# Performance work log

Hardware: AMD Instinct MI355X
Metric: run time of the kernel (lower is better)

Reference implementation:

```python
import jax, jax.numpy as jnp
import numpy as np

N_IMG = 256; N_PAD = 512; N_DELAYS = 32; N_GRID = 512
PIX = 4e-5; L_IMG = N_IMG * PIX
R_BODY = 0.008; V0 = 1500.0; GRID_HALF = 0.02
N_TH = 240; N_INT = 250; W0 = 30.0
LAM_TV = 1e-3; LAM_L1 = 1e-3

def _fourier_coord(n, l):
    f = np.fft.fftshift(np.fft.fftfreq(n, d=l / n))
    kx, ky = np.meshgrid(f, f, indexing='ij')
    k = 2.0 * np.pi * np.sqrt(kx ** 2 + ky ** 2)
    theta = np.mod(np.arctan2(ky, kx), 2.0 * np.pi)
    return k.astype(np.float32), theta.astype(np.float32)

_K2D, _TH2D = _fourier_coord(N_PAD, 2.0 * L_IMG)
K2D = jnp.asarray(_K2D)[None, None]            # [1,1,P,P]
TH2D = jnp.asarray(_TH2D)                      # [P,P]
MASK0 = jnp.asarray(((_TH2D >= 0.0) & (_TH2D <= 2 * np.pi)).astype(np.float32))
_THPI = np.mod(_TH2D + np.pi, 2 * np.pi)
MASK1 = jnp.asarray(((_THPI >= 0.0) & (_THPI <= 2 * np.pi)).astype(np.float32))
K_LOSS = jnp.asarray(np.fft.ifftshift(_K2D))[None, None]
_SIG = 0.0015 / PIX / np.sqrt(2.0 * np.log(2.0))   # gaussian window sigma (pixels)
_AX = np.arange(N_IMG) - (N_IMG - 1) / 2.0
_G = np.exp(-_AX ** 2 / (2.0 * _SIG ** 2))
GWIN = jnp.asarray(np.outer(_G, _G).astype(np.float32))[None]   # [1,N,N]
THETAS_WF = jnp.linspace(0.0, 2.0 * np.pi, N_TH, dtype=jnp.float32)   # [T]
STEPS = jnp.linspace(0.0, 1.0, N_INT, dtype=jnp.float32)[None]        # [1,S]


def _interp1d(xg, yg, xn):
    # linear interp on uniform grid xg (1D) of values yg; xn arbitrary shape
    dxg = xg[1] - xg[0]
    t = (xn - xg[0]) / dxg
    f = jnp.clip(jnp.floor(t).astype(jnp.int32), 0, xg.shape[0] - 1)
    c = jnp.clip(jnp.ceil(t).astype(jnp.int32), 0, xg.shape[0] - 1)
    yf, yc = yg[f], yg[c]
    denom = jnp.where(c == f, 1.0, xg[c] - xg[f])
    lin = yf + (yc - yf) * (xn - xg[f]) / denom
    return jnp.where(c == f, yc, lin)


def _wavefront(xq, yq, SoS, x_vec, y_vec):
    # time-of-flight wavefront: trapezoid quadrature of (1 - v0/SoS) along rays
    r = jnp.sqrt(xq ** 2 + yq ** 2)
    phi = jnp.arctan2(xq, yq)
    th = THETAS_WF[:, None]                      # [T,1]
    s = jnp.sin(th - phi)
    cd = jnp.cos(th - phi)                       # cos(phi - th) == cos(th - phi)
    disc = jnp.maximum(R_BODY ** 2 - (r * s) ** 2, 0.0)
    l_in = jnp.sqrt(disc) + r * cd
    l_out = 2.0 * jnp.sqrt(disc) * (cd >= 0.0).astype(jnp.float32)
    l = jnp.where(r < R_BODY, l_in, l_out)       # [T,1]
    dx = x_vec[1] - x_vec[0]
    dy = y_vec[1] - y_vec[0]
    xi = jnp.round((xq - l * STEPS * jnp.sin(th) - x_vec[0]) / dx).astype(jnp.int32)
    yi = jnp.round((yq - l * STEPS * jnp.cos(th) - y_vec[0]) / dy).astype(jnp.int32)
    fint = 1.0 - V0 / SoS[(-yi) % N_GRID, xi % N_GRID]   # [T,S] gather
    xs = l * STEPS                               # [T,S]
    wf = jnp.sum(0.5 * (fint[:, 1:] + fint[:, :-1]) * (xs[:, 1:] - xs[:, :-1]), axis=1)
    return THETAS_WF, wf


def _tf_pact(delays, thetas, wfs):
    w = _interp1d(thetas, wfs, TH2D)
    w_pi = _interp1d(thetas, wfs, jnp.mod(TH2D + jnp.pi, 2.0 * jnp.pi))
    d = delays.reshape(1, -1, 1, 1)
    tf = (jnp.exp(-1j * K2D * (d - w)) * MASK0 + jnp.exp(1j * K2D * (d - w_pi)) * MASK1) * 0.5
    return jnp.fft.ifftshift(tf, axes=(-2, -1))  # [1,D,P,P] complex


def _siren(x, W1, b1, W2, b2, W3, b3, W4, b4):
    h = jnp.sin(W0 * (x @ W1 + b1))
    h = jnp.sin(W0 * (h @ W2 + b2))
    h = jnp.sin(W0 * (h @ W3 + b3))
    return h @ W4 + b4


def _forward(W1, b1, W2, b2, W3, b3, W4, b4, y_img, delays, xq, yq,
             mgrid_masked, mask, mask_idx, x_vec, y_vec):
    out = _siren(mgrid_masked, W1, b1, W2, b2, W3, b3, W4, b4)[:, 0]
    SoS = jnp.full((N_GRID * N_GRID,), 1499.363, jnp.float32)
    SoS = SoS.at[mask_idx].set(out * 170.0 + 1550.0).reshape(N_GRID, N_GRID)
    thetas, wfs = _wavefront(xq[0], yq[0], SoS, x_vec, y_vec)
    H = _tf_pact(delays, thetas, wfs)
    yw = y_img * GWIN                                  # [1,D,N,N]
    pad = N_IMG // 2
    yp = jnp.pad(yw, ((0, 0), (0, 0), (pad, pad), (pad, pad)))
    Y = jnp.fft.fft2(jnp.fft.ifftshift(yp, axes=(-2, -1)))
    Ht = jnp.conj(H)
    HtH = jnp.abs(H) ** 2
    rhs = jnp.sum(Y * Ht, axis=-3, keepdims=True)
    lhs = jnp.sum(HtH, axis=-3, keepdims=True)
    X = rhs / lhs
    x_rec = jnp.fft.fftshift(jnp.fft.ifft2(X), axes=(-2, -1)).real
    data = jnp.mean((jnp.abs(Y) * K_LOSS - jnp.abs(H * X) * K_LOSS) ** 2, axis=(-3, -2, -1))
    tv = LAM_TV * (jnp.sum(jnp.abs((SoS[1:, :] - SoS[:-1, :]) * mask[1:, :]))
                   + jnp.sum(jnp.abs((SoS[:, 1:] - SoS[:, :-1]) * mask[:, 1:])))
    l1 = LAM_L1 * jnp.mean(jnp.abs(SoS - 1550.0) * mask)
    loss = data + tv + l1
    return x_rec, SoS, loss


def setup_inputs() -> dict:
    key = jax.random.key(0)
    ks = jax.random.split(key, 12)
    xg = np.linspace(-GRID_HALF, GRID_HALF, N_GRID).astype(np.float32)
    XX, YY = np.meshgrid(xg, xg, indexing='ij')
    mask_np = (XX ** 2 + YY ** 2 <= R_BODY ** 2).astype(np.float32)
    mask_idx = np.nonzero(mask_np.reshape(-1))[0].astype(np.int32)
    lin = np.linspace(-1.0, 1.0, N_GRID).astype(np.float32)
    GX, GY = np.meshgrid(lin, lin, indexing='ij')
    mgrid = np.stack([GX, GY], axis=-1).reshape(-1, 2)
    H = 128
    c = np.sqrt(6.0 / H) / W0
    def u(k, shape, b):
        return jax.random.uniform(k, shape, jnp.float32, -b, b)
    return {
        'W1': u(ks[0], (2, H), 0.5), 'b1': u(ks[1], (H,), 0.5),
        'W2': u(ks[2], (H, H), c), 'b2': u(ks[3], (H,), c),
        'W3': u(ks[4], (H, H), c), 'b3': u(ks[5], (H,), c),
        'W4': u(ks[6], (H, 1), c), 'b4': u(ks[7], (1,), c),
        'y_img': jax.random.normal(ks[8], (1, N_DELAYS, N_IMG, N_IMG), jnp.float32),
        'delays': jax.random.normal(ks[9], (N_DELAYS,), jnp.float32) * 5e-4,
        'xq': jnp.array([0.002], jnp.float32),
        'yq': jnp.array([0.001], jnp.float32),
        'mgrid_masked': jnp.asarray(mgrid[mask_idx]),
        'mask': jnp.asarray(mask_np),
        'mask_idx': jnp.asarray(mask_idx),
        'x_vec': jnp.asarray(xg),
        'y_vec': jnp.asarray(xg),
    }


def reference(W1, b1, W2, b2, W3, b3, W4, b4, y_img, delays, xq, yq,
              mgrid_masked, mask, mask_idx, x_vec, y_vec):
    return _forward(W1, b1, W2, b2, W3, b3, W4, b4, y_img, delays, xq, yq,
                    mgrid_masked, mask, mask_idx, x_vec, y_vec)
```

## Files before the change

### kernel.cpp

```cpp
#include <hip/hip_runtime.h>
#include <hip/hip_bf16.h>
#include <math.h>

#define NP 512
#define NIMG 256
#define NDEL 32
#define NTH 240
#define NINT 250
#define SOS_ELEMS (512*512)
#define MLP_P 32
#define PHY(i) ((i) + ((i) >> 3))
#define RSW 576
#define PI_F 3.14159265358979323846f

__device__ __forceinline__ int brev9(int i) { return (int)(__brev((unsigned)i) >> 23); }

__device__ __forceinline__ float block_reduce_any(float v) {
  #pragma unroll
  for (int o = 32; o > 0; o >>= 1) v += __shfl_down(v, o, 64);
  __shared__ float red[16];
  int lane = threadIdx.x & 63, wid = threadIdx.x >> 6;
  __syncthreads();
  if (lane == 0) red[wid] = v;
  __syncthreads();
  float r = 0.f;
  if (threadIdx.x == 0) {
    int nw = blockDim.x >> 6;
    for (int i = 0; i < nw; ++i) r += red[i];
  }
  return r;
}

__device__ __forceinline__ void r4_bfly(float2& x0, float2& x1, float2& x2, float2& x3,
                                        float c1, float s1n, float c2, float s2n, float sign) {
  float t1x = x1.x * c1 - x1.y * s1n, t1y = x1.x * s1n + x1.y * c1;
  float y0x = x0.x + t1x, y0y = x0.y + t1y;
  float y1x = x0.x - t1x, y1y = x0.y - t1y;
  float t3x = x3.x * c1 - x3.y * s1n, t3y = x3.x * s1n + x3.y * c1;
  float y2x = x2.x + t3x, y2y = x2.y + t3y;
  float y3x = x2.x - t3x, y3y = x2.y - t3y;
  float t2x = y2x * c2 - y2y * s2n, t2y = y2x * s2n + y2y * c2;
  float ux = y3x * c2 - y3y * s2n, uy = y3x * s2n + y3y * c2;
  float t4x = -sign * uy, t4y = sign * ux;
  x0 = make_float2(y0x + t2x, y0y + t2y);
  x2 = make_float2(y0x - t2x, y0y - t2y);
  x1 = make_float2(y1x + t4x, y1y + t4y);
  x3 = make_float2(y1x - t4x, y1y - t4y);
}

__device__ __forceinline__ void fft512_r4_fwd_rows(float2 (*s)[RSW], int lt) {
  #pragma unroll
  for (int pass = 0; pass < 4; ++pass) {
    const int sh = 2 * pass;
    const int h = 1 << sh;
    int p = lt & 127;
    int rbase = (lt >> 7) << 2;
    int j = p & (h - 1);
    int g = p >> sh;
    int base = (g << (sh + 2)) + j;
    int i0 = PHY(base), i1 = PHY(base + h), i2 = PHY(base + 2 * h), i3 = PHY(base + 3 * h);
    float ang1 = -PI_F * (float)j / (float)h;
    float s1n, c1; __sincosf(ang1, &s1n, &c1);
    float s2n, c2; __sincosf(0.5f * ang1, &s2n, &c2);
    #pragma unroll
    for (int rr = 0; rr < 4; ++rr) {
      int r = rbase + rr;
      float2 x0 = s[r][i0], x1 = s[r][i1], x2 = s[r][i2], x3 = s[r][i3];
      r4_bfly(x0, x1, x2, x3, c1, s1n, c2, s2n, -1.f);
      s[r][i0] = x0; s[r][i1] = x1; s[r][i2] = x2; s[r][i3] = x3;
    }
    __syncthreads();
  }
  {
    int p = lt;
    int i1 = PHY(p), i2 = PHY(p + 256);
    float ang = -PI_F * (float)p * (1.f / 256.f);
    float sn, cs; __sincosf(ang, &sn, &cs);
    #pragma unroll
    for (int r = 0; r < 8; ++r) {
      float2 a = s[r][i1], b = s[r][i2];
      float tr = b.x * cs - b.y * sn;
      float ti = b.x * sn + b.y * cs;
      s[r][i1] = make_float2(a.x + tr, a.y + ti);
      s[r][i2] = make_float2(a.x - tr, a.y - ti);
    }
    __syncthreads();
  }
}

__device__ __forceinline__ void fft512_r4_fwd_rows4(float2 (*s)[RSW], int tid) {
  #pragma unroll
  for (int pass = 0; pass < 4; ++pass) {
    const int sh = 2 * pass;
    const int h = 1 << sh;
    int p = tid & 127;
    int rbase = (tid >> 7) << 1;
    int j = p & (h - 1);
    int g = p >> sh;
    int base = (g << (sh + 2)) + j;
    int i0 = PHY(base), i1 = PHY(base + h), i2 = PHY(base + 2 * h), i3 = PHY(base + 3 * h);
    float ang1 = -PI_F * (float)j / (float)h;
    float s1n, c1; __sincosf(ang1, &s1n, &c1);
    float s2n, c2; __sincosf(0.5f * ang1, &s2n, &c2);
    #pragma unroll
    for (int rr = 0; rr < 2; ++rr) {
      int r = rbase + rr;
      float2 x0 = s[r][i0], x1 = s[r][i1], x2 = s[r][i2], x3 = s[r][i3];
      r4_bfly(x0, x1, x2, x3, c1, s1n, c2, s2n, -1.f);
      s[r][i0] = x0; s[r][i1] = x1; s[r][i2] = x2; s[r][i3] = x3;
    }
    __syncthreads();
  }
  {
    int p = tid;
    int i1 = PHY(p), i2 = PHY(p + 256);
    float ang = -PI_F * (float)p * (1.f / 256.f);
    float sn, cs; __sincosf(ang, &sn, &cs);
    #pragma unroll
    for (int r = 0; r < 4; ++r) {
      float2 a = s[r][i1], b = s[r][i2];
      float tr = b.x * cs - b.y * sn;
      float ti = b.x * sn + b.y * cs;
      s[r][i1] = make_float2(a.x + tr, a.y + ti);
      s[r][i2] = make_float2(a.x - tr, a.y - ti);
    }
    __syncthreads();
  }
}

__device__ __forceinline__ void fft512_r4_row(float2* s, int tid, float sign) {
  #pragma unroll
  for (int pass = 0; pass < 4; ++pass) {
    const int sh = 2 * pass;
    const int h = 1 << sh;
    if (tid < 128) {
      int j = tid & (h - 1);
      int g = tid >> sh;
      int base = (g << (sh + 2)) + j;
      int i0 = PHY(base), i1 = PHY(base + h), i2 = PHY(base + 2 * h), i3 = PHY(base + 3 * h);
      float ang1 = sign * PI_F * (float)j / (float)h;
      float s1n, c1; __sincosf(ang1, &s1n, &c1);
      float s2n, c2; __sincosf(0.5f * ang1, &s2n, &c2);
      float2 x0 = s[i0], x1 = s[i1], x2 = s[i2], x3 = s[i3];
      r4_bfly(x0, x1, x2, x3, c1, s1n, c2, s2n, sign);
      s[i0] = x0; s[i1] = x1; s[i2] = x2; s[i3] = x3;
    }
    __syncthreads();
  }
  {
    int i1 = PHY(tid), i2 = PHY(tid + 256);
    float ang = sign * PI_F * (float)tid * (1.f / 256.f);
    float sn, cs; __sincosf(ang, &sn, &cs);
    float2 a = s[i1], b = s[i2];
    float tr = b.x * cs - b.y * sn;
    float ti = b.x * sn + b.y * cs;
    s[i1] = make_float2(a.x + tr, a.y + ti);
    s[i2] = make_float2(a.x - tr, a.y - ti);
    __syncthreads();
  }
}

__global__ __launch_bounds__(256) void k_front(
    const float* __restrict__ W1, const float* __restrict__ b1,
    const float* __restrict__ W2, const float* __restrict__ b2,
    const float* __restrict__ W3, const float* __restrict__ b3,
    const float* __restrict__ W4v, const float* __restrict__ b4,
    const float* __restrict__ mgrid, const int* __restrict__ mask_idx,
    const float* __restrict__ mask, int M, int nMlpB,
    float* __restrict__ sos, float* __restrict__ acc,
    const float* __restrict__ y_img, float2* __restrict__ bufA) {
  __shared__ char raw[43008];
  int bid = blockIdx.x;
  int tid = threadIdx.x;
  if (bid < nMlpB) {
    float (*hbuf)[MLP_P][132] = (float (*)[MLP_P][132])raw;
    float (*wbuf)[8][132]     = (float (*)[8][132])(raw + 33792);
    float (*xy2)[2]           = (float (*)[2])(raw + 33792 + 8448);
    int half = tid >> 7, lt = tid & 127;
    int base = bid * (2 * MLP_P) + half * MLP_P;
    if (lt < MLP_P * 2) {
      int p = lt >> 1, c = lt & 1;
      float v = 0.f;
      if (base + p < M) v = mgrid[(base + p) * 2 + c];
      xy2[half * MLP_P + p][c] = v;
    }
    if (bid == 0 && tid < 4) acc[tid] = 0.f;
    for (int slab = bid; slab < 1024; slab += nMlpB) {
      int t = slab * 256 + tid;
      if (mask[t] == 0.f) sos[t] = 1499.363f;
    }
    __syncthreads();
    for (int e = lt; e < MLP_P * 128; e += 128) {
      int p = e >> 7, j = e & 127;
      hbuf[half][p][j] = __sinf(30.f * (xy2[half * MLP_P + p][0] * W1[j] +
                                        xy2[half * MLP_P + p][1] * W1[128 + j] + b1[j]));
    }
    __syncthreads();

    int jg = lt & 15, pg = lt >> 4;
    int jA = jg * 4, jB = 64 + jg * 4;
    int p0 = pg * 4;
    int wr = tid >> 4, wc = (tid & 15) << 3;
    #pragma unroll
    for (int layer = 0; layer < 2; ++layer) {
      const float* Wg = layer ? W3 : W2;
      const float* bb = layer ? b3 : b2;
      float acr[4][8];
      #pragma unroll
      for (int i = 0; i < 4; ++i)
        #pragma unroll
        for (int j = 0; j < 8; ++j) acr[i][j] = 0.f;

      float4 pre1, pre2;
      if (tid < 128) {
        pre1 = *(const float4*)&Wg[wr * 128 + wc];
        pre2 = *(const float4*)&Wg[wr * 128 + wc + 4];
      }
      for (int c = 0; c < 16; ++c) {
        if (tid < 128) {
          *(float4*)&wbuf[c & 1][wr][wc] = pre1;
          *(float4*)&wbuf[c & 1][wr][wc + 4] = pre2;
        }
        __syncthreads();
        if (tid < 128 && c < 15) {
          pre1 = *(const float4*)&Wg[((c + 1) * 8 + wr) * 128 + wc];
          pre2 = *(const float4*)&Wg[((c + 1) * 8 + wr) * 128 + wc + 4];
        }
        int k0 = c * 8;
        float hreg[4][8];
        #pragma unroll
        for (int i = 0; i < 4; ++i) {
          float4 ha = *(const float4*)&hbuf[half][p0 + i][k0];
          float4 hb = *(const float4*)&hbuf[half][p0 + i][k0 + 4];
          hreg[i][0] = ha.x; hreg[i][1] = ha.y; hreg[i][2] = ha.z; hreg[i][3] = ha.w;
          hreg[i][4] = hb.x; hreg[i][5] = hb.y; hreg[i][6] = hb.z; hreg[i][7] = hb.w;
        }
        #pragma unroll
        for (int kk = 0; kk < 8; ++kk) {
          float4 wa = *(const float4*)&wbuf[c & 1][kk][jA];
          float4 wb = *(const float4*)&wbuf[c & 1][kk][jB];
          float w8[8] = {wa.x, wa.y, wa.z, wa.w, wb.x, wb.y, wb.z, wb.w};
          #pragma unroll
          for (int i = 0; i < 4; ++i) {
            float hv = hreg[i][kk];
            #pragma unroll
            for (int j = 0; j < 8; ++j) acr[i][j] += hv * w8[j];
          }
        }
      }
      float breg[8];
      #pragma unroll
      for (int j = 0; j < 4; ++j) { breg[j] = bb[jA + j]; breg[4 + j] = bb[jB + j]; }
      __syncthreads();
      #pragma unroll
      for (int i = 0; i < 4; ++i) {
        float o[8];
        #pragma unroll
        for (int j = 0; j < 8; ++j) o[j] = __sinf(30.f * (acr[i][j] + breg[j]));
        *(float4*)&hbuf[half][p0 + i][jA] = make_float4(o[0], o[1], o[2], o[3]);
        *(float4*)&hbuf[half][p0 + i][jB] = make_float4(o[4], o[5], o[6], o[7]);
      }
      __syncthreads();
    }
    {
      int p = lt >> 2, q = lt & 3;
      float s = 0.f;
      #pragma unroll
      for (int k = 0; k < 32; k += 4) {
        float4 h4 = *(const float4*)&hbuf[half][p][q * 32 + k];
        float4 w4 = *(const float4*)&W4v[q * 32 + k];
        s += h4.x * w4.x + h4.y * w4.y + h4.z * w4.z + h4.w * w4.w;
      }
      s += __shfl_down(s, 1, 64);
      s += __shfl_down(s, 2, 64);
      if (q == 0 && base + p < M)
        sos[mask_idx[base + p]] = (s + b4[0]) * 170.f + 1550.f;
    }
  } else {
    float2 (*s)[RSW] = (float2 (*)[RSW])raw;
    int fb = bid - nMlpB;
    int rt = fb & 31;
    int d = fb >> 5;
    const float INV2S2 = (float)(0.6931471805599453 / 1406.25);
    for (int e = tid; e < 2048; e += 256) {
      int i = e >> 8, c = e & 255;
      int r = rt * 8 + i;
      float axr = (float)r - 127.5f;
      float axc = (float)c - 127.5f;
      float g = __expf(-(axr * axr + axc * axc) * INV2S2);
      float val = y_img[((size_t)d << 16) + (r << 8) + c] * g;
      int p = i >> 1, comp = i & 1;
      ((float*)&s[p][PHY(brev9((c + 384) & 511))])[comp] = val;
      ((float*)&s[p][PHY(brev9(c + 128))])[comp] = 0.f;
    }
    __syncthreads();
    fft512_r4_fwd_rows4(s, tid);
    float2* outp = bufA + ((size_t)d << 17) + rt * 8;
    for (int e = tid; e < 2056; e += 256) {
      int i = e & 7, v = e >> 3;
      int p = i >> 1, comp = i & 1;
      float2 Zv = s[p][PHY(v)];
      float2 Zm = s[p][PHY((512 - v) & 511)];
      float2 Yv;
      if (comp == 0) Yv = make_float2(0.5f * (Zv.x + Zm.x), 0.5f * (Zv.y - Zm.y));
      else           Yv = make_float2(0.5f * (Zv.y + Zm.y), 0.5f * (Zm.x - Zv.x));
      outp[(size_t)v * 256 + i] = Yv;
    }
  }
}

__global__ __launch_bounds__(256) void k_side(
    const float* __restrict__ sos, const float* __restrict__ xq_p,
    const float* __restrict__ yq_p, const float* __restrict__ x_vec,
    const float* __restrict__ y_vec, float* __restrict__ wfs) {
  int i = blockIdx.x;
  int j = threadIdx.x;
  float xq = xq_p[0], yq = yq_p[0];
  float r = sqrtf(xq * xq + yq * yq);
  float phi = atan2f(xq, yq);
  float th = (float)((double)i * (2.0 * M_PI / 239.0));
  float sn = sinf(th - phi), cd = cosf(th - phi);
  const float R2 = 0.008f * 0.008f;
  float disc = fmaxf(R2 - (r * sn) * (r * sn), 0.f);
  float sq = sqrtf(disc);
  float l_in = sq + r * cd;
  float l_out = 2.f * sq * (cd >= 0.f ? 1.f : 0.f);
  float l = (r < 0.008f) ? l_in : l_out;
  float x0 = x_vec[0], dx = x_vec[1] - x_vec[0];
  float y0 = y_vec[0], dy = y_vec[1] - y_vec[0];
  float sinth = sinf(th), costh = cosf(th);
  float contrib = 0.f;
  if (j < NINT) {
    float sj = (float)j * (1.f / 249.f);
    int xi = (int)rintf((xq - l * sj * sinth - x0) / dx);
    int yi = (int)rintf((yq - l * sj * costh - y0) / dy);
    float sv = sos[(((-yi) & 511) << 9) + (xi & 511)];
    float f = 1.f - 1500.f / sv;
    float wgt = (j == 0 || j == NINT - 1) ? 0.5f : 1.f;
    contrib = wgt * f;
  }
  float tot = block_reduce_any(contrib);
  if (threadIdx.x == 0) wfs[i] = tot * l * (1.f / 249.f);
}

__device__ __forceinline__ float interp_wf(const float* wfs, float xn) {
  const float dxg = (float)(2.0 * M_PI / 239.0);
  float t = xn / dxg;
  int f = (int)floorf(t); f = min(max(f, 0), 239);
  int c = (int)ceilf(t);  c = min(max(c, 0), 239);
  float yf = wfs[f], yc = wfs[c];
  if (c == f) return yc;
  float xgf = (float)f * dxg;
  return yf + (yc - yf) * (xn - xgf) / ((float)(c - f) * dxg);
}

__global__ __launch_bounds__(256) void k_colfft_part(
    float2* bufA,
    const float* __restrict__ delays, const float* __restrict__ wfs_g,
    const float* __restrict__ sos, const float* __restrict__ mask,
    float* __restrict__ acc) {
  __shared__ float2 s[8][RSW];
  __shared__ float wfs[NTH];
  __shared__ float dly[8];
  int b = blockIdx.x;
  int tid = threadIdx.x;
  if (b >= 1028) {
    int t = (b - 1028) * 256 + tid;
    float sv = sos[t];
    float m = mask[t];
    int i = t >> 9, j = t & 511;
    float tv = 0.f;
    if (i > 0) tv += fabsf((sv - sos[t - 512]) * m);
    if (j > 0) tv += fabsf((sv - sos[t - 1]) * m);
    float l1 = fabsf(sv - 1550.f) * m;
    float tvb = block_reduce_any(tv);
    float l1b = block_reduce_any(l1);
    if (tid == 0) {
      atomicAdd(&acc[1], tvb);
      atomicAdd(&acc[2], l1b);
    }
    return;
  }
  int v = b >> 2;
  int h = b & 3;
  if (tid < NTH) wfs[tid] = wfs_g[tid];
  if (tid < 8) dly[tid] = delays[h * 8 + tid];
  __syncthreads();

  const float inv_nd = 1.f / 0.02048f;
  const float TWO_PI = 6.28318530717958647692f;
  float fy = (float)(v < 256 ? v : v - 512) * inv_nd;
  float kkA[2];
  float2 zw[2], zwpi[2];
  int up[2];
  #pragma unroll
  for (int uu = 0; uu < 2; ++uu) {
    int u = tid + 256 * uu;
    up[uu] = PHY(u);
    float fx = (float)(u < 256 ? u : u - 512) * inv_nd;
    float kk = TWO_PI * sqrtf(fx * fx + fy * fy);
    kkA[uu] = kk;
    float th = atan2f(fy, fx);
    if (th < 0.f) th += TWO_PI;
    float w = interp_wf(wfs, th);
    float thpi = th + PI_F;
    if (thpi >= TWO_PI) thpi -= TWO_PI;
    float wpi = interp_wf(wfs, thpi);
    float snw, csw; __sincosf(kk * w, &snw, &csw);
    zw[uu] = make_float2(csw, snw);
    float snp, csp; __sincosf(kk * wpi, &snp, &csp);
    zwpi[uu] = make_float2(csp, snp);
  }

  for (int e = tid; e < 2048; e += 256) {
    int ch = e >> 8, c = e & 255;
    float2 val = bufA[((size_t)(h * 8 + ch) << 17) + (size_t)v * 256 + c];
    s[ch][PHY(brev9((c + 384) & 511))] = val;
    s[ch][PHY(brev9(c + 128))] = make_float2(0.f, 0.f);
  }
  __syncthreads();
  fft512_r4_fwd_rows(s, tid);

  float rhsr[2] = {0.f, 0.f}, rhsi[2] = {0.f, 0.f}, lhs[2] = {0.f, 0.f};
  float sY2[2] = {0.f, 0.f}, sYH[2] = {0.f, 0.f};
  #pragma unroll
  for (int uu = 0; uu < 2; ++uu) {
    float kk = kkA[uu];
    float2 w0 = zw[uu], w1 = zwpi[uu];
    #pragma unroll
    for (int ch = 0; ch < 8; ++ch) {
      float dl = dly[ch];
      float sd, cd2;
      __sincosf(kk * dl, &sd, &cd2);
      float t0r = cd2 * w0.x + sd * w0.y;
      float t0i = cd2 * w0.y - sd * w0.x;
      float t1r = cd2 * w1.x + sd * w1.y;
      float t1i = sd * w1.x - cd2 * w1.y;
      float Hr = 0.5f * (t0r + t1r);
      float Hi = 0.5f * (t0i + t1i);
      float2 Yv = s[ch][up[uu]];
      rhsr[uu] += Yv.x * Hr + Yv.y * Hi;
      rhsi[uu] += Yv.y * Hr - Yv.x * Hi;
      float h2 = Hr * Hr + Hi * Hi;
      float y2 = Yv.x * Yv.x + Yv.y * Yv.y;
      lhs[uu] += h2;
      sY2[uu] += y2;
      sYH[uu] += sqrtf(y2 * h2);
    }
  }

  float lw = (v == 0 || v == 256) ? 1.f : 2.f;
  float lsum = kkA[0] * kkA[0] * sY2[0] + kkA[1] * kkA[1] * sY2[1];
  float bs = block_reduce_any(lsum * lw);
  if (tid == 0) atomicAdd(&acc[0], bs);

  float* fb = (float*)bufA;
  #pragma unroll
  for (int uu = 0; uu < 2; ++uu) {
    int u = tid + 256 * uu;
    size_t base = ((size_t)v << 9) + u;
    fb[(((size_t)(h * 8 + 0)) << 18) + base] = rhsr[uu];
    fb[(((size_t)(h * 8 + 1)) << 18) + base] = rhsi[uu];
    fb[(((size_t)(h * 8 + 2)) << 18) + base] = lhs[uu];
    fb[(((size_t)(h * 8 + 3)) << 18) + base] = sYH[uu];
  }
}

__global__ __launch_bounds__(256) void k_colfft_fin(
    const float* __restrict__ bufP, float2* __restrict__ Xo,
    float* __restrict__ acc) {
  __shared__ float2 s[RSW];
  int v = blockIdx.x;
  int tid = threadIdx.x;
  const float inv_nd = 1.f / 0.02048f;
  const float TWO_PI = 6.28318530717958647692f;
  float fy = (float)(v < 256 ? v : v - 512) * inv_nd;
  float lw = (v == 0 || v == 256) ? 1.f : 2.f;
  float lsum = 0.f;
  float2 Xv[2];
  #pragma unroll
  for (int uu = 0; uu < 2; ++uu) {
    int u = tid + 256 * uu;
    float fx = (float)(u < 256 ? u : u - 512) * inv_nd;
    float kk2 = TWO_PI * TWO_PI * (fx * fx + fy * fy);
    float R = 0.f, I = 0.f, L = 0.f, YH = 0.f;
    size_t base = ((size_t)v << 9) + u;
    #pragma unroll
    for (int h = 0; h < 4; ++h) {
      R  += bufP[(((size_t)(h * 8 + 0)) << 18) + base];
      I  += bufP[(((size_t)(h * 8 + 1)) << 18) + base];
      L  += bufP[(((size_t)(h * 8 + 2)) << 18) + base];
      YH += bufP[(((size_t)(h * 8 + 3)) << 18) + base];
    }
    float Xr = R / L, Xi = I / L;
    Xv[uu] = make_float2(Xr, Xi);
    float aX = sqrtf(Xr * Xr + Xi * Xi);
    lsum += kk2 * (aX * aX * L - 2.f * aX * YH);
  }
  float bs = block_reduce_any(lsum * lw);
  if (tid == 0) atomicAdd(&acc[0], bs);

  s[PHY(brev9(tid))] = Xv[0];
  s[PHY(brev9(tid + 256))] = Xv[1];
  __syncthreads();
  fft512_r4_row(s, tid, +1.f);
  const float sc = 1.f / 512.f;
  float2 o0 = s[PHY(tid)], o1 = s[PHY(tid + 256)];
  o0.x *= sc; o0.y *= sc; o1.x *= sc; o1.y *= sc;
  Xo[((size_t)tid << 9) + v] = o0;
  Xo[((size_t)(tid + 256) << 9) + v] = o1;
  if (v != 0 && v != 256) {
    int vm = 512 - v;
    Xo[((size_t)tid << 9) + vm] = make_float2(o0.x, -o0.y);
    Xo[((size_t)(tid + 256) << 9) + vm] = make_float2(o1.x, -o1.y);
  }
}

__global__ __launch_bounds__(256) void k_final_rows(const float2* __restrict__ buf,
                                                    float* __restrict__ xrec,
                                                    const float* __restrict__ acc,
                                                    float* __restrict__ lossout) {
  __shared__ float2 s[RSW];
  int arow = blockIdx.x;
  const float2* p = buf + ((size_t)arow << 9);
  int tid = threadIdx.x;
  if (arow == 0 && tid == 0)
    lossout[0] = acc[0] * (1.f / 8388608.f) + 1e-3f * acc[1] + 1e-3f * (acc[2] * (1.f / 262144.f));
  s[PHY(brev9(tid))] = p[tid];
  s[PHY(brev9(tid + 256))] = p[tid + 256];
  __syncthreads();
  fft512_r4_row(s, tid, +1.f);
  int orow = (arow + 256) & 511;
  const float sc = 1.f / 512.f;
  xrec[(orow << 9) + ((tid + 256) & 511)] = s[PHY(tid)].x * sc;
  xrec[(orow << 9) + (tid & 511)] = s[PHY(tid + 256)].x * sc;
}

extern "C" void kernel_launch(void* const* d_in, const int* in_sizes, int n_in,
                              void* d_out, int out_size, void* d_ws, size_t ws_size,
                              hipStream_t stream) {
  const float* W1 = (const float*)d_in[0];
  const float* b1 = (const float*)d_in[1];
  const float* W2 = (const float*)d_in[2];
  const float* b2 = (const float*)d_in[3];
  const float* W3 = (const float*)d_in[4];
  const float* b3 = (const float*)d_in[5];
  const float* W4 = (const float*)d_in[6];
  const float* b4 = (const float*)d_in[7];
  const float* y_img = (const float*)d_in[8];
  const float* delays = (const float*)d_in[9];
  const float* xq = (const float*)d_in[10];
  const float* yq = (const float*)d_in[11];
  const float* mgrid = (const float*)d_in[12];
  const float* mask = (const float*)d_in[13];
  const int* mask_idx = (const int*)d_in[14];
  const float* x_vec = (const float*)d_in[15];
  const float* y_vec = (const float*)d_in[16];
  const int M = in_sizes[14];
  const int nMlpB = (M + 2 * MLP_P - 1) / (2 * MLP_P);

  float* out = (float*)d_out;
  float* xrec = out;
  float* sos = out + SOS_ELEMS;
  float* loss = out + 2 * SOS_ELEMS;

  char* wsb = (char*)d_ws;
  float* acc = (float*)wsb;
  float* wfs = (float*)(wsb + 1024);
  float2* bufA = (float2*)(wsb + 4096);
  float2* bufX = (float2*)(wsb + 4096 + (size_t)NDEL * 512 * 256 * sizeof(float2));

  k_front<<<nMlpB + 1024, 256, 0, stream>>>(W1, b1, W2, b2, W3, b3, W4, b4,
                                            mgrid, mask_idx, mask, M, nMlpB,
                                            sos, acc, y_img, bufA);
  k_side<<<NTH, 256, 0, stream>>>(sos, xq, yq, x_vec, y_vec, wfs);
  k_colfft_part<<<1028 + 1024, 256, 0, stream>>>(bufA, delays, wfs, sos, mask, acc);
  k_colfft_fin<<<257, 256, 0, stream>>>((const float*)bufA, bufX, acc);
  k_final_rows<<<512, 256, 0, stream>>>(bufX, xrec, acc, loss);
}
```

Before: 203.6 us.

## Swizzle colfft shared layout, spread loss atomics, reorder TV blocks first

The padded shared-memory layout (PHY, 576 columns) in the column-FFT kernel becomes an XOR swizzle on 512 columns. The wavefront table and reduction scratch now live in that same buffer, and the delays move into registers, which cuts LDS use per block and may raise occupancy. Loss accumulators are split across 16 slots per term, each on its own 64-byte line, to reduce atomic contention, and the final kernel sums the slots. The TV/L1 blocks are moved to the front of the grid. The risk is that the swizzle brings back LDS bank conflicts on some FFT passes.

Measured after the change: 181.1 us. 1.12x faster.

```diff
diff --git a/kernel.cpp b/kernel.cpp
--- a/kernel.cpp
+++ b/kernel.cpp
@@ -11,6 +11,7 @@
 #define MLP_P 32
 #define PHY(i) ((i) + ((i) >> 3))
 #define RSW 576
+#define SWZ(i) ((i) ^ (((i) >> 6) & 7))
 #define PI_F 3.14159265358979323846f
 
 __device__ __forceinline__ int brev9(int i) { return (int)(__brev((unsigned)i) >> 23); }
@@ -27,6 +28,21 @@
   if (threadIdx.x == 0) {
     int nw = blockDim.x >> 6;
     for (int i = 0; i < nw; ++i) r += red[i];
+  }
+  return r;
+}
+
+__device__ __forceinline__ float block_reduce_scratch(float v, float* scratch) {
+  #pragma unroll
+  for (int o = 32; o > 0; o >>= 1) v += __shfl_down(v, o, 64);
+  int lane = threadIdx.x & 63, wid = threadIdx.x >> 6;
+  __syncthreads();
+  if (lane == 0) scratch[wid] = v;
+  __syncthreads();
+  float r = 0.f;
+  if (threadIdx.x == 0) {
+    #pragma unroll
+    for (int i = 0; i < 4; ++i) r += scratch[i];
   }
   return r;
 }
@@ -48,7 +64,7 @@
   x3 = make_float2(y1x - t4x, y1y - t4y);
 }
 
-__device__ __forceinline__ void fft512_r4_fwd_rows(float2 (*s)[RSW], int lt) {
+__device__ __forceinline__ void fft512_r4_fwd_rows_swz(float2 (*s)[512], int lt) {
   #pragma unroll
   for (int pass = 0; pass < 4; ++pass) {
     const int sh = 2 * pass;
@@ -58,7 +74,7 @@
     int j = p & (h - 1);
     int g = p >> sh;
     int base = (g << (sh + 2)) + j;
-    int i0 = PHY(base), i1 = PHY(base + h), i2 = PHY(base + 2 * h), i3 = PHY(base + 3 * h);
+    int i0 = SWZ(base), i1 = SWZ(base + h), i2 = SWZ(base + 2 * h), i3 = SWZ(base + 3 * h);
     float ang1 = -PI_F * (float)j / (float)h;
     float s1n, c1; __sincosf(ang1, &s1n, &c1);
     float s2n, c2; __sincosf(0.5f * ang1, &s2n, &c2);
@@ -73,7 +89,7 @@
   }
   {
     int p = lt;
-    int i1 = PHY(p), i2 = PHY(p + 256);
+    int i1 = SWZ(p), i2 = SWZ(p + 256);
     float ang = -PI_F * (float)p * (1.f / 256.f);
     float sn, cs; __sincosf(ang, &sn, &cs);
     #pragma unroll
@@ -159,6 +175,8 @@
     __syncthreads();
   }
 }
+
+#define ACC_G(g, slot) ((g) * 256 + ((slot) & 15) * 16)
 
 __global__ __launch_bounds__(256) void k_front(
     const float* __restrict__ W1, const float* __restrict__ b1,
@@ -184,7 +202,9 @@
       if (base + p < M) v = mgrid[(base + p) * 2 + c];
       xy2[half * MLP_P + p][c] = v;
     }
-    if (bid == 0 && tid < 4) acc[tid] = 0.f;
+    if (bid == 0) {
+      for (int e = tid; e < 768; e += 256) acc[e] = 0.f;
+    }
     for (int slab = bid; slab < 1024; slab += nMlpB) {
       int t = slab * 256 + tid;
       if (mask[t] == 0.f) sos[t] = 1499.363f;
@@ -359,13 +379,12 @@
     const float* __restrict__ delays, const float* __restrict__ wfs_g,
     const float* __restrict__ sos, const float* __restrict__ mask,
     float* __restrict__ acc) {
-  __shared__ float2 s[8][RSW];
-  __shared__ float wfs[NTH];
-  __shared__ float dly[8];
+  __shared__ float2 s[8][512];
   int b = blockIdx.x;
   int tid = threadIdx.x;
-  if (b >= 1028) {
-    int t = (b - 1028) * 256 + tid;
+  float* scratch = (float*)&s[0][0];
+  if (b < 1024) {
+    int t = b * 256 + tid;
     float sv = sos[t];
     float m = mask[t];
     int i = t >> 9, j = t & 511;
@@ -373,18 +392,22 @@
     if (i > 0) tv += fabsf((sv - sos[t - 512]) * m);
     if (j > 0) tv += fabsf((sv - sos[t - 1]) * m);
     float l1 = fabsf(sv - 1550.f) * m;
-    float tvb = block_reduce_any(tv);
-    float l1b = block_reduce_any(l1);
+    float tvb = block_reduce_scratch(tv, scratch);
+    float l1b = block_reduce_scratch(l1, scratch + 8);
     if (tid == 0) {
-      atomicAdd(&acc[1], tvb);
-      atomicAdd(&acc[2], l1b);
+      atomicAdd(&acc[ACC_G(1, b)], tvb);
+      atomicAdd(&acc[ACC_G(2, b)], l1b);
     }
     return;
   }
-  int v = b >> 2;
-  int h = b & 3;
-  if (tid < NTH) wfs[tid] = wfs_g[tid];
-  if (tid < 8) dly[tid] = delays[h * 8 + tid];
+  int job = b - 1024;
+  int v = job >> 2;
+  int h = job & 3;
+
+  if (tid < NTH) scratch[tid] = wfs_g[tid];
+  float dreg[8];
+  #pragma unroll
+  for (int ch = 0; ch < 8; ++ch) dreg[ch] = delays[h * 8 + ch];
   __syncthreads();
 
   const float inv_nd = 1.f / 0.02048f;
@@ -392,34 +415,33 @@
   float fy = (float)(v < 256 ? v : v - 512) * inv_nd;
   float kkA[2];
   float2 zw[2], zwpi[2];
-  int up[2];
   #pragma unroll
   for (int uu = 0; uu < 2; ++uu) {
     int u = tid + 256 * uu;
-    up[uu] = PHY(u);
     float fx = (float)(u < 256 ? u : u - 512) * inv_nd;
     float kk = TWO_PI * sqrtf(fx * fx + fy * fy);
     kkA[uu] = kk;
     float th = atan2f(fy, fx);
     if (th < 0.f) th += TWO_PI;
-    float w = interp_wf(wfs, th);
+    float w = interp_wf(scratch, th);
     float thpi = th + PI_F;
     if (thpi >= TWO_PI) thpi -= TWO_PI;
-    float wpi = interp_wf(wfs, thpi);
+    float wpi = interp_wf(scratch, thpi);
     float snw, csw; __sincosf(kk * w, &snw, &csw);
     zw[uu] = make_float2(csw, snw);
     float snp, csp; __sincosf(kk * wpi, &snp, &csp);
     zwpi[uu] = make_float2(csp, snp);
   }
+  __syncthreads();
 
   for (int e = tid; e < 2048; e += 256) {
     int ch = e >> 8, c = e & 255;
     float2 val = bufA[((size_t)(h * 8 + ch) << 17) + (size_t)v * 256 + c];
-    s[ch][PHY(brev9((c + 384) & 511))] = val;
-    s[ch][PHY(brev9(c + 128))] = make_float2(0.f, 0.f);
-  }
-  __syncthreads();
-  fft512_r4_fwd_rows(s, tid);
+    s[ch][SWZ(brev9((c + 384) & 511))] = val;
+    s[ch][SWZ(brev9(c + 128))] = make_float2(0.f, 0.f);
+  }
+  __syncthreads();
+  fft512_r4_fwd_rows_swz(s, tid);
 
   float rhsr[2] = {0.f, 0.f}, rhsi[2] = {0.f, 0.f}, lhs[2] = {0.f, 0.f};
   float sY2[2] = {0.f, 0.f}, sYH[2] = {0.f, 0.f};
@@ -427,9 +449,10 @@
   for (int uu = 0; uu < 2; ++uu) {
     float kk = kkA[uu];
     float2 w0 = zw[uu], w1 = zwpi[uu];
+    int u = SWZ(tid + 256 * uu);
     #pragma unroll
     for (int ch = 0; ch < 8; ++ch) {
-      float dl = dly[ch];
+      float dl = dreg[ch];
       float sd, cd2;
       __sincosf(kk * dl, &sd, &cd2);
       float t0r = cd2 * w0.x + sd * w0.y;
@@ -438,7 +461,7 @@
       float t1i = sd * w1.x - cd2 * w1.y;
       float Hr = 0.5f * (t0r + t1r);
       float Hi = 0.5f * (t0i + t1i);
-      float2 Yv = s[ch][up[uu]];
+      float2 Yv = s[ch][u];
       rhsr[uu] += Yv.x * Hr + Yv.y * Hi;
       rhsi[uu] += Yv.y * Hr - Yv.x * Hi;
       float h2 = Hr * Hr + Hi * Hi;
@@ -450,9 +473,9 @@
   }
 
   float lw = (v == 0 || v == 256) ? 1.f : 2.f;
-  float lsum = kkA[0] * kkA[0] * sY2[0] + kkA[1] * kkA[1] * sY2[1];
-  float bs = block_reduce_any(lsum * lw);
-  if (tid == 0) atomicAdd(&acc[0], bs);
+  float lsum = (kkA[0] * kkA[0] * sY2[0] + kkA[1] * kkA[1] * sY2[1]) * lw;
+  float bs = block_reduce_scratch(lsum, scratch);
+  if (tid == 0) atomicAdd(&acc[ACC_G(0, job)], bs);
 
   float* fb = (float*)bufA;
   #pragma unroll
@@ -498,7 +521,7 @@
     lsum += kk2 * (aX * aX * L - 2.f * aX * YH);
   }
   float bs = block_reduce_any(lsum * lw);
-  if (tid == 0) atomicAdd(&acc[0], bs);
+  if (tid == 0) atomicAdd(&acc[ACC_G(0, v)], bs);
 
   s[PHY(brev9(tid))] = Xv[0];
   s[PHY(brev9(tid + 256))] = Xv[1];
@@ -524,8 +547,16 @@
   int arow = blockIdx.x;
   const float2* p = buf + ((size_t)arow << 9);
   int tid = threadIdx.x;
-  if (arow == 0 && tid == 0)
-    lossout[0] = acc[0] * (1.f / 8388608.f) + 1e-3f * acc[1] + 1e-3f * (acc[2] * (1.f / 262144.f));
+  if (arow == 0 && tid == 0) {
+    float a0 = 0.f, a1 = 0.f, a2 = 0.f;
+    #pragma unroll
+    for (int i = 0; i < 16; ++i) {
+      a0 += acc[ACC_G(0, i)];
+      a1 += acc[ACC_G(1, i)];
+      a2 += acc[ACC_G(2, i)];
+    }
+    lossout[0] = a0 * (1.f / 8388608.f) + 1e-3f * a1 + 1e-3f * (a2 * (1.f / 262144.f));
+  }
   s[PHY(brev9(tid))] = p[tid];
   s[PHY(brev9(tid + 256))] = p[tid + 256];
   __syncthreads();
@@ -566,7 +597,7 @@
 
   char* wsb = (char*)d_ws;
   float* acc = (float*)wsb;
-  float* wfs = (float*)(wsb + 1024);
+  float* wfs = (float*)(wsb + 3072);
   float2* bufA = (float2*)(wsb + 4096);
   float2* bufX = (float2*)(wsb + 4096 + (size_t)NDEL * 512 * 256 * sizeof(float2));
 
@@ -574,7 +605,7 @@
                                             mgrid, mask_idx, mask, M, nMlpB,
                                             sos, acc, y_img, bufA);
   k_side<<<NTH, 256, 0, stream>>>(sos, xq, yq, x_vec, y_vec, wfs);
-  k_colfft_part<<<1028 + 1024, 256, 0, stream>>>(bufA, delays, wfs, sos, mask, acc);
+  k_colfft_part<<<1024 + 1028, 256, 0, stream>>>(bufA, delays, wfs, sos, mask, acc);
   k_colfft_fin<<<257, 256, 0, stream>>>((const float*)bufA, bufX, acc);
   k_final_rows<<<512, 256, 0, stream>>>(bufX, xrec, acc, loss);
 }
```
